# Optimization experiments

Measured on AMD Instinct MI355X. Metric: run time of the kernel, lower is better.

## Reference

```python
import jax, jax.numpy as jnp
import numpy as np

ALPHA = 1.702
LIMIT = 7.0


def setup_inputs() -> dict:
    key = jax.random.key(0)
    ks = jax.random.split(key, 7)
    B, S, H, I, E, K = 1, 512, 2880, 2880, 8, 4
    T = B * S
    return {
        "hidden_states": jax.random.normal(ks[0], (B, S, H), jnp.float32),
        "router_indices": jax.random.randint(ks[1], (T, K), 0, E),
        "routing_weights": jax.random.uniform(ks[2], (T, E), jnp.float32),
        "gate_up_proj": jax.random.normal(ks[3], (E, H, 2 * I), jnp.float32) * 0.02,
        "gate_up_proj_bias": jax.random.normal(ks[4], (E, 2 * I), jnp.float32) * 0.02,
        "down_proj": jax.random.normal(ks[5], (E, I, H), jnp.float32) * 0.02,
        "down_proj_bias": jax.random.normal(ks[6], (E, H), jnp.float32) * 0.02,
    }


def reference(hidden_states, router_indices, routing_weights,
              gate_up_proj, gate_up_proj_bias, down_proj, down_proj_bias):
    B, S, H = hidden_states.shape
    E = routing_weights.shape[1]
    x = hidden_states.reshape(-1, H)  # [T, H]

    # How many of the top-k slots of each token selected expert e.
    # (index_add_ in the torch code adds once per matching slot.)
    counts = jnp.sum(
        router_indices[:, :, None] == jnp.arange(E)[None, None, :], axis=1
    ).astype(x.dtype)  # [T, E]
    combine = routing_weights * counts  # [T, E]

    # Per-expert gate/up projection: [E, T, 2I]
    gate_up = jnp.einsum('th,ehf->etf', x, gate_up_proj) + gate_up_proj_bias[:, None, :]
    gate = jnp.minimum(gate_up[..., ::2], LIMIT)           # clamp(max=limit)
    up = jnp.clip(gate_up[..., 1::2], -LIMIT, LIMIT)       # clamp(+-limit)
    glu = gate * jax.nn.sigmoid(gate * ALPHA)
    h = (up + 1.0) * glu                                   # [E, T, I]

    # Per-expert down projection then weighted scatter-add combine.
    out = jnp.einsum('eti,eih->eth', h, down_proj) + down_proj_bias[:, None, :]
    y = jnp.einsum('te,eth->th', combine, out)             # [T, H]
    return y.reshape(B, S, H)
```

## Files before the change

kernel.cpp:

```cpp
#include <hip/hip_runtime.h>
#include <stdint.h>

#define ALPHA 1.702f
#define LIMIT 7.0f

constexpr int T_TOK = 512;
constexpr int HDIM  = 2880;
constexpr int IDIM  = 2880;
constexpr int NEXP  = 8;
constexpr int GUDIM = 2 * IDIM;
constexpr int CAP   = 512;
constexpr int KDIM  = 2880;

constexpr int BM = 256;
constexpr int BN = 64;
constexpr int BK = 32;

typedef __attribute__((ext_vector_type(8))) short s16x8;
typedef __attribute__((ext_vector_type(4))) float f32x4;

__device__ __forceinline__ uint32_t pack2_bf16(float a, float b) {
  union { float f; uint32_t u; } x, y;
  x.f = a; y.f = b;
  uint32_t ra = (x.u + 0x7FFFu + ((x.u >> 16) & 1u)) >> 16;
  uint32_t rb = (y.u + 0x7FFFu + ((y.u >> 16) & 1u)) >> 16;
  return ra | (rb << 16);
}

__device__ __forceinline__ uint16_t f2bf(float f) {
  union { float f; uint32_t u; } x; x.f = f;
  return (uint16_t)((x.u + 0x7FFFu + ((x.u >> 16) & 1u)) >> 16);
}

__device__ __forceinline__ void async_copy16(const void* g, void* l) {
  typedef __attribute__((address_space(1))) const uint32_t* gp_t;
  typedef __attribute__((address_space(3))) uint32_t* lp_t;
  __builtin_amdgcn_global_load_lds((gp_t)g, (lp_t)l, 16, 0, 0);
}

__global__ void routing_kernel(const int* __restrict__ ridx,
                               const float* __restrict__ rw,
                               int* __restrict__ mcount,
                               int* __restrict__ tok,
                               float* __restrict__ comb) {
  __shared__ int cnt[NEXP];
  const int t = threadIdx.x;
  if (t < NEXP) cnt[t] = 0;
  __syncthreads();
  if (t < T_TOK) {
    const int i0 = ridx[t * 4 + 0], i1 = ridx[t * 4 + 1];
    const int i2 = ridx[t * 4 + 2], i3 = ridx[t * 4 + 3];
#pragma unroll
    for (int e = 0; e < NEXP; ++e) {
      int c = (i0 == e) + (i1 == e) + (i2 == e) + (i3 == e);
      if (c) {
        int p = atomicAdd(&cnt[e], 1);
        tok[e * CAP + p]  = t;
        comb[e * CAP + p] = rw[t * NEXP + e] * (float)c;
      }
    }
  }
  __syncthreads();
  if (t < NEXP) mcount[t] = cnt[t];
}

__global__ void gather_kernel(const float* __restrict__ x,
                              const int* __restrict__ mcount,
                              const int* __restrict__ tok,
                              uint32_t* __restrict__ Apack) {
  const int m = blockIdx.x;
  const int e = blockIdx.y;
  if (m >= mcount[e]) return;
  const int t = tok[e * CAP + m];
  const float* src = x + (size_t)t * HDIM;
  uint32_t* dst = Apack + (size_t)(e * CAP + m) * (HDIM / 2);
  for (int c = threadIdx.x * 4; c < HDIM; c += 1024) {
    float4 v = *(const float4*)(src + c);
    uint2 p = make_uint2(pack2_bf16(v.x, v.y), pack2_bf16(v.z, v.w));
    *(uint2*)(dst + c / 2) = p;
  }
}

template <bool IS_GATEUP, int NDIM>
__global__ __launch_bounds__(512) void moe_gemm(
    const uint16_t* __restrict__ A,
    const float* __restrict__ W,
    const float* __restrict__ bias,
    const int* __restrict__ mcount,
    const int* __restrict__ tok,
    const float* __restrict__ comb,
    uint16_t* __restrict__ Hout,
    float* __restrict__ yout)
{
  const int e = blockIdx.z;
  const int M = mcount[e];
  const int m_base = blockIdx.y * BM;
  if (m_base >= M) return;
  const int n_base = blockIdx.x * BN;

  __shared__ uint16_t lA[BM * BK];
  __shared__ uint16_t lB[BN * BK];

  const int tid  = threadIdx.x;
  const int wid  = tid >> 6;
  const int lane = tid & 63;
  const int wm = wid >> 1;
  const int wn = wid & 1;

  f32x4 acc[4][2];
#pragma unroll
  for (int i = 0; i < 4; ++i)
#pragma unroll
    for (int j = 0; j < 2; ++j)
      acc[i][j] = f32x4{0.f, 0.f, 0.f, 0.f};

  const uint16_t* aP = A + ((size_t)e * CAP + m_base + wid * 32 + (lane >> 2)) * KDIM
                         + (lane & 3) * 8;
  uint16_t* lA0 = &lA[(wid * 32) * BK];
  uint16_t* lA1 = &lA[(wid * 32 + 16) * BK];

  const int bn  = tid & 63;
  const int bkq = tid >> 6;
  const float* wP = W + (size_t)e * KDIM * NDIM + (size_t)(bkq * 4) * NDIM + n_base + bn;
  uint32_t* lBw = (uint32_t*)&lB[bn * BK + bkq * 4];

  const int aRd0 = (wm * 64 + (lane & 15)) * BK + (lane >> 4) * 8;
  const int bRd0 = (wn * 32 + (lane & 15)) * BK + (lane >> 4) * 8;

  for (int kk = 0; kk < KDIM / BK; ++kk) {
    __syncthreads();
    async_copy16(aP, lA0);
    async_copy16(aP + 16 * KDIM, lA1);
    float v0 = wP[0];
    float v1 = wP[(size_t)NDIM];
    float v2 = wP[(size_t)2 * NDIM];
    float v3 = wP[(size_t)3 * NDIM];
    uint32_t p0 = pack2_bf16(v0, v1);
    uint32_t p1 = pack2_bf16(v2, v3);
    lBw[0] = p0;
    lBw[1] = p1;
    aP += BK;
    wP += (size_t)BK * NDIM;
    __syncthreads();

    s16x8 af[4], bfr[2];
#pragma unroll
    for (int mt = 0; mt < 4; ++mt)
      af[mt] = *(const s16x8*)&lA[aRd0 + mt * 16 * BK];
#pragma unroll
    for (int nt = 0; nt < 2; ++nt)
      bfr[nt] = *(const s16x8*)&lB[bRd0 + nt * 16 * BK];
#pragma unroll
    for (int mt = 0; mt < 4; ++mt)
#pragma unroll
      for (int nt = 0; nt < 2; ++nt)
        acc[mt][nt] = __builtin_amdgcn_mfma_f32_16x16x32_bf16(
            af[mt], bfr[nt], acc[mt][nt], 0, 0, 0);
  }

  const int col0 = n_base + wn * 32 + (lane & 15);
  const float b0 = bias[e * NDIM + col0];
  const float b1 = bias[e * NDIM + col0 + 16];

  if (IS_GATEUP) {
#pragma unroll
    for (int mt = 0; mt < 4; ++mt) {
      const int rbase = m_base + wm * 64 + mt * 16 + ((lane >> 4) << 2);
#pragma unroll
      for (int r = 0; r < 4; ++r) {
        float v0 = acc[mt][0][r] + b0;
        float v1 = acc[mt][1][r] + b1;
        float o0 = __shfl_xor(v0, 1, 64);
        float o1 = __shfl_xor(v1, 1, 64);
        int rr = rbase + r;
        if (rr < M && (lane & 1) == 0) {
          float g0 = fminf(v0, LIMIT);
          float u0 = fminf(fmaxf(o0, -LIMIT), LIMIT);
          float h0 = (u0 + 1.f) * (g0 / (1.f + __expf(-ALPHA * g0)));
          float g1 = fminf(v1, LIMIT);
          float u1 = fminf(fmaxf(o1, -LIMIT), LIMIT);
          float h1 = (u1 + 1.f) * (g1 / (1.f + __expf(-ALPHA * g1)));
          uint16_t* dst = Hout + ((size_t)e * CAP + rr) * IDIM;
          dst[col0 >> 1]        = f2bf(h0);
          dst[(col0 + 16) >> 1] = f2bf(h1);
        }
      }
    }
  } else {
#pragma unroll
    for (int mt = 0; mt < 4; ++mt) {
      const int rbase = m_base + wm * 64 + mt * 16 + ((lane >> 4) << 2);
#pragma unroll
      for (int r = 0; r < 4; ++r) {
        int rr = rbase + r;
        if (rr < M) {
          int t = tok[e * CAP + rr];
          float cw = comb[e * CAP + rr];
          float* yp = yout + (size_t)t * HDIM;
          atomicAdd(yp + col0,      cw * (acc[mt][0][r] + b0));
          atomicAdd(yp + col0 + 16, cw * (acc[mt][1][r] + b1));
        }
      }
    }
  }
}

extern "C" void kernel_launch(void* const* d_in, const int* in_sizes, int n_in,
                              void* d_out, int out_size, void* d_ws, size_t ws_size,
                              hipStream_t stream) {
  const float* x    = (const float*)d_in[0];
  const int*   ridx = (const int*)d_in[1];
  const float* rw   = (const float*)d_in[2];
  const float* w_gu = (const float*)d_in[3];
  const float* b_gu = (const float*)d_in[4];
  const float* w_dn = (const float*)d_in[5];
  const float* b_dn = (const float*)d_in[6];
  float* y = (float*)d_out;

  char* ws = (char*)d_ws;
  int*      mcount = (int*)ws;
  int*      tok    = (int*)(ws + 256);
  float*    comb   = (float*)(ws + 256 + NEXP * CAP * 4);
  uint16_t* Apack  = (uint16_t*)(ws + 256 + 2 * NEXP * CAP * 4);
  uint16_t* Hbuf   = Apack + (size_t)NEXP * CAP * KDIM;

  hipMemsetAsync(y, 0, (size_t)T_TOK * HDIM * sizeof(float), stream);
  routing_kernel<<<1, 512, 0, stream>>>(ridx, rw, mcount, tok, comb);
  gather_kernel<<<dim3(CAP, NEXP), 256, 0, stream>>>(x, mcount, tok, (uint32_t*)Apack);
  moe_gemm<true, GUDIM><<<dim3(GUDIM / BN, 2, NEXP), 512, 0, stream>>>(
      Apack, w_gu, b_gu, mcount, tok, comb, Hbuf, y);
  moe_gemm<false, HDIM><<<dim3(HDIM / BN, 2, NEXP), 512, 0, stream>>>(
      Hbuf, w_dn, b_dn, mcount, tok, comb, (uint16_t*)nullptr, y);
}
```

Measured before the change: 1.095 ms.

## Load A fragments directly from global and double-buffer W tiles with register prefetch

Removes the A tile staging through LDS: each wave now reads its A MFMA fragments straight from global memory. The fp32 weight tile is prefetched two K-steps ahead into registers and packed to bf16 into a padded, double-buffered LDS tile, so there is one barrier per K-step instead of two. It also adds a min-blocks-per-SM launch bound. This aims to overlap weight loads with MFMA work and cut LDS traffic and synchronisation, at the cost of uncoalesced A reads from global and more register pressure.

```diff
diff --git a/kernel.cpp b/kernel.cpp
--- a/kernel.cpp
+++ b/kernel.cpp
@@ -15,6 +15,7 @@
 constexpr int BM = 256;
 constexpr int BN = 64;
 constexpr int BK = 32;
+constexpr int RS = 34;
 
 typedef __attribute__((ext_vector_type(8))) short s16x8;
 typedef __attribute__((ext_vector_type(4))) float f32x4;
@@ -30,12 +31,6 @@
 __device__ __forceinline__ uint16_t f2bf(float f) {
   union { float f; uint32_t u; } x; x.f = f;
   return (uint16_t)((x.u + 0x7FFFu + ((x.u >> 16) & 1u)) >> 16);
-}
-
-__device__ __forceinline__ void async_copy16(const void* g, void* l) {
-  typedef __attribute__((address_space(1))) const uint32_t* gp_t;
-  typedef __attribute__((address_space(3))) uint32_t* lp_t;
-  __builtin_amdgcn_global_load_lds((gp_t)g, (lp_t)l, 16, 0, 0);
 }
 
 __global__ void routing_kernel(const int* __restrict__ ridx,
@@ -82,7 +77,7 @@
 }
 
 template <bool IS_GATEUP, int NDIM>
-__global__ __launch_bounds__(512) void moe_gemm(
+__global__ __launch_bounds__(512, 4) void moe_gemm(
     const uint16_t* __restrict__ A,
     const float* __restrict__ W,
     const float* __restrict__ bias,
@@ -98,8 +93,7 @@
   if (m_base >= M) return;
   const int n_base = blockIdx.x * BN;
 
-  __shared__ uint16_t lA[BM * BK];
-  __shared__ uint16_t lB[BN * BK];
+  __shared__ uint16_t lB[2][BN * RS];
 
   const int tid  = threadIdx.x;
   const int wid  = tid >> 6;
@@ -114,48 +108,93 @@
     for (int j = 0; j < 2; ++j)
       acc[i][j] = f32x4{0.f, 0.f, 0.f, 0.f};
 
-  const uint16_t* aP = A + ((size_t)e * CAP + m_base + wid * 32 + (lane >> 2)) * KDIM
-                         + (lane & 3) * 8;
-  uint16_t* lA0 = &lA[(wid * 32) * BK];
-  uint16_t* lA1 = &lA[(wid * 32 + 16) * BK];
+  const uint16_t* aF0 = A + ((size_t)e * CAP + m_base + wm * 64 + (lane & 15)) * KDIM
+                          + (lane >> 4) * 8;
+  const uint16_t* aF1 = aF0 + (size_t)16 * KDIM;
+  const uint16_t* aF2 = aF0 + (size_t)32 * KDIM;
+  const uint16_t* aF3 = aF0 + (size_t)48 * KDIM;
 
   const int bn  = tid & 63;
   const int bkq = tid >> 6;
-  const float* wP = W + (size_t)e * KDIM * NDIM + (size_t)(bkq * 4) * NDIM + n_base + bn;
-  uint32_t* lBw = (uint32_t*)&lB[bn * BK + bkq * 4];
-
-  const int aRd0 = (wm * 64 + (lane & 15)) * BK + (lane >> 4) * 8;
-  const int bRd0 = (wn * 32 + (lane & 15)) * BK + (lane >> 4) * 8;
-
-  for (int kk = 0; kk < KDIM / BK; ++kk) {
-    __syncthreads();
-    async_copy16(aP, lA0);
-    async_copy16(aP + 16 * KDIM, lA1);
-    float v0 = wP[0];
-    float v1 = wP[(size_t)NDIM];
-    float v2 = wP[(size_t)2 * NDIM];
-    float v3 = wP[(size_t)3 * NDIM];
-    uint32_t p0 = pack2_bf16(v0, v1);
-    uint32_t p1 = pack2_bf16(v2, v3);
-    lBw[0] = p0;
-    lBw[1] = p1;
-    aP += BK;
-    wP += (size_t)BK * NDIM;
-    __syncthreads();
-
-    s16x8 af[4], bfr[2];
-#pragma unroll
-    for (int mt = 0; mt < 4; ++mt)
-      af[mt] = *(const s16x8*)&lA[aRd0 + mt * 16 * BK];
-#pragma unroll
-    for (int nt = 0; nt < 2; ++nt)
-      bfr[nt] = *(const s16x8*)&lB[bRd0 + nt * 16 * BK];
-#pragma unroll
-    for (int mt = 0; mt < 4; ++mt)
-#pragma unroll
-      for (int nt = 0; nt < 2; ++nt)
-        acc[mt][nt] = __builtin_amdgcn_mfma_f32_16x16x32_bf16(
-            af[mt], bfr[nt], acc[mt][nt], 0, 0, 0);
+  const int wOff = bn * RS + bkq * 4;
+  const size_t wStep = (size_t)BK * NDIM;
+  const float* wP0 = W + (size_t)e * KDIM * NDIM + (size_t)(bkq * 4) * NDIM + n_base + bn;
+
+  const int bRd0 = (wn * 32 + (lane & 15)) * RS + (lane >> 4) * 8;
+  const int bRd1 = bRd0 + 16 * RS;
+
+  constexpr int NK = KDIM / BK;
+
+  float p00, p01, p02, p03, p10, p11, p12, p13;
+  p00 = wP0[0];
+  p01 = wP0[(size_t)NDIM];
+  p02 = wP0[2 * (size_t)NDIM];
+  p03 = wP0[3 * (size_t)NDIM];
+  {
+    const float* w1 = wP0 + wStep;
+    p10 = w1[0];
+    p11 = w1[(size_t)NDIM];
+    p12 = w1[2 * (size_t)NDIM];
+    p13 = w1[3 * (size_t)NDIM];
+  }
+  const float* wP = wP0 + 2 * wStep;
+  {
+    uint32_t* wd = (uint32_t*)&lB[0][wOff];
+    wd[0] = pack2_bf16(p00, p01);
+    wd[1] = pack2_bf16(p02, p03);
+  }
+  __syncthreads();
+
+  for (int kk = 0; kk < NK; kk += 2) {
+#pragma unroll
+    for (int u = 0; u < 2; ++u) {
+      s16x8 af0 = *(const s16x8*)aF0;
+      s16x8 af1 = *(const s16x8*)aF1;
+      s16x8 af2 = *(const s16x8*)aF2;
+      s16x8 af3 = *(const s16x8*)aF3;
+      aF0 += BK; aF1 += BK; aF2 += BK; aF3 += BK;
+
+      const int k = kk + u;
+      const bool ld = (k + 2 < NK);
+      const float* wq = ld ? wP : wP0;
+      float n0 = wq[0];
+      float n1 = wq[(size_t)NDIM];
+      float n2 = wq[2 * (size_t)NDIM];
+      float n3 = wq[3 * (size_t)NDIM];
+      if (ld) wP += wStep;
+
+      union { uint32_t w[4]; s16x8 v; } b0, b1;
+      {
+        const uint32_t* r0 = (const uint32_t*)&lB[u][bRd0];
+        const uint32_t* r1 = (const uint32_t*)&lB[u][bRd1];
+        b0.w[0] = r0[0]; b0.w[1] = r0[1]; b0.w[2] = r0[2]; b0.w[3] = r0[3];
+        b1.w[0] = r1[0]; b1.w[1] = r1[1]; b1.w[2] = r1[2]; b1.w[3] = r1[3];
+      }
+
+      acc[0][0] = __builtin_amdgcn_mfma_f32_16x16x32_bf16(af0, b0.v, acc[0][0], 0, 0, 0);
+      acc[0][1] = __builtin_amdgcn_mfma_f32_16x16x32_bf16(af0, b1.v, acc[0][1], 0, 0, 0);
+      acc[1][0] = __builtin_amdgcn_mfma_f32_16x16x32_bf16(af1, b0.v, acc[1][0], 0, 0, 0);
+      acc[1][1] = __builtin_amdgcn_mfma_f32_16x16x32_bf16(af1, b1.v, acc[1][1], 0, 0, 0);
+      acc[2][0] = __builtin_amdgcn_mfma_f32_16x16x32_bf16(af2, b0.v, acc[2][0], 0, 0, 0);
+      acc[2][1] = __builtin_amdgcn_mfma_f32_16x16x32_bf16(af2, b1.v, acc[2][1], 0, 0, 0);
+      acc[3][0] = __builtin_amdgcn_mfma_f32_16x16x32_bf16(af3, b0.v, acc[3][0], 0, 0, 0);
+      acc[3][1] = __builtin_amdgcn_mfma_f32_16x16x32_bf16(af3, b1.v, acc[3][1], 0, 0, 0);
+
+      {
+        uint32_t* wd = (uint32_t*)&lB[1 - u][wOff];
+        if (u == 0) {
+          wd[0] = pack2_bf16(p10, p11);
+          wd[1] = pack2_bf16(p12, p13);
+          p00 = n0; p01 = n1; p02 = n2; p03 = n3;
+        } else {
+          wd[0] = pack2_bf16(p00, p01);
+          wd[1] = pack2_bf16(p02, p03);
+          p10 = n0; p11 = n1; p12 = n2; p13 = n3;
+        }
+      }
+
+      asm volatile("s_waitcnt lgkmcnt(0)\n\ts_barrier" ::: "memory");
+    }
   }
 
   const int col0 = n_base + wn * 32 + (lane & 15);
```

After: 1.320 ms. 20.6% more time.
